# Optimization experiments

Measured on AMD Instinct MI355X. Metric: run time of the kernel, lower is better.

Reference implementation:

```python
import jax, jax.numpy as jnp
import numpy as np

B, S, D_MODEL, HEAD, D_KV = 8, 1024, 1024, 16, 64


def setup_inputs() -> dict:
    key = jax.random.key(0)
    ks = jax.random.split(key, 10)
    std = 1.0 / np.sqrt(D_MODEL)
    inp = {
        "queries": jax.random.normal(ks[0], (B, S, D_MODEL), jnp.float32),
        "keys": jax.random.normal(ks[1], (B, S, D_MODEL), jnp.float32),
        "values": jax.random.normal(ks[2], (B, S, D_MODEL), jnp.float32),
        "group_prob": jax.random.uniform(ks[3], (B, 1, S, S), jnp.float32),
        "attention_mask": jax.random.randint(ks[4], (B, 1, S, S), 0, 2, jnp.int32),
        "Wq": jax.random.normal(ks[5], (HEAD * D_KV, D_MODEL), jnp.float32) * std,
        "bq": jnp.zeros((HEAD * D_KV,), jnp.float32),
        "Wk": jax.random.normal(ks[6], (HEAD * D_KV, D_MODEL), jnp.float32) * std,
        "bk": jnp.zeros((HEAD * D_KV,), jnp.float32),
        "Wv": jax.random.normal(ks[7], (HEAD * D_KV, D_MODEL), jnp.float32) * std,
        "bv": jnp.zeros((HEAD * D_KV,), jnp.float32),
    }
    return inp


def reference(queries, keys, values, group_prob, attention_mask, Wq, bq, Wk, bk, Wv, bv):
    b, nq = queries.shape[:2]
    # QKV projections -> [b, head, seq, d_kv]
    q = (queries @ Wq.T + bq).reshape(b, nq, HEAD, D_KV).transpose(0, 2, 1, 3)
    k = (keys @ Wk.T + bk).reshape(b, -1, HEAD, D_KV).transpose(0, 2, 1, 3)
    v = (values @ Wv.T + bv).reshape(b, -1, HEAD, D_KV).transpose(0, 2, 1, 3)
    # scaled scores [b, head, nq, nk]
    att = jnp.einsum("bhqd,bhkd->bhqk", q, k) / np.sqrt(D_KV).astype(np.float32)
    # NOTE: the original torch code calls att.masked_fill(...) (out-of-place)
    # and discards the result, so attention_mask has no effect. Replicated here.
    att = jax.nn.softmax(att, axis=-1)
    att = att * group_prob  # post-softmax group scaling (breaks fused SDPA)
    out = jnp.einsum("bhqk,bhkd->bhqd", att, v)
    return out.transpose(0, 2, 1, 3).reshape(b, nq, HEAD * D_KV)
```

## Files before the change

kernel.cpp:

```cpp
#include <hip/hip_runtime.h>

#define B_SZ 8
#define S_SZ 1024
#define DM   1024
#define NH   16
#define DK   64

typedef __bf16 bf16;
typedef __bf16 bf16x8 __attribute__((ext_vector_type(8)));
typedef float  f32x4  __attribute__((ext_vector_type(4)));

__device__ __forceinline__ f32x4 mfma16x16x32(bf16x8 a, bf16x8 b, f32x4 c) {
    return __builtin_amdgcn_mfma_f32_16x16x32_bf16(a, b, c, 0, 0, 0);
}

typedef const __attribute__((address_space(1))) void* gptr_t;
typedef __attribute__((address_space(3))) void*       sptr_t;
__device__ __forceinline__ void async_cp16(const void* g, void* s) {
    __builtin_amdgcn_global_load_lds((gptr_t)g, (sptr_t)s, 16, 0, 0);
}

__global__ __launch_bounds__(256)
void cvt_kernel(const float* __restrict__ x0, const float* __restrict__ x1,
                const float* __restrict__ x2, const float* __restrict__ w0,
                const float* __restrict__ w1, const float* __restrict__ w2,
                bf16* __restrict__ xb, bf16* __restrict__ wb)
{
    const int z = blockIdx.y;
    const float* src;
    bf16* dst;
    int n;
    if (z < 3) {
        src = (z == 0) ? x0 : (z == 1) ? x1 : x2;
        dst = xb + (size_t)z * (8u * 1024 * 1024);
        n = 8 * 1024 * 1024;
    } else {
        const int w = z - 3;
        src = (w == 0) ? w0 : (w == 1) ? w1 : w2;
        dst = wb + (size_t)w * (1024 * 1024);
        n = 1024 * 1024;
    }
    const int idx = (blockIdx.x * 256 + threadIdx.x) * 8;
    if (idx >= n) return;
    const float4 a = *(const float4*)(src + idx);
    const float4 c = *(const float4*)(src + idx + 4);
    union { bf16 h[8]; uint4 u; } pk;
    pk.h[0] = (bf16)a.x; pk.h[1] = (bf16)a.y; pk.h[2] = (bf16)a.z; pk.h[3] = (bf16)a.w;
    pk.h[4] = (bf16)c.x; pk.h[5] = (bf16)c.y; pk.h[6] = (bf16)c.z; pk.h[7] = (bf16)c.w;
    *(uint4*)(dst + idx) = pk.u;
}

__global__ __launch_bounds__(256)
void cvt_gp_kernel(const float* __restrict__ gp, bf16* __restrict__ gpb)
{
    const int idx = (blockIdx.x * 256 + threadIdx.x) * 8;
    const float4 a = *(const float4*)(gp + idx);
    const float4 c = *(const float4*)(gp + idx + 4);
    union { bf16 h[8]; uint4 u; } pk;
    pk.h[0] = (bf16)a.x; pk.h[1] = (bf16)a.y; pk.h[2] = (bf16)a.z; pk.h[3] = (bf16)a.w;
    pk.h[4] = (bf16)c.x; pk.h[5] = (bf16)c.y; pk.h[6] = (bf16)c.z; pk.h[7] = (bf16)c.w;
    *(uint4*)(gpb + idx) = pk.u;
}

__global__ __launch_bounds__(256, 2)
void qkv_gemm(const bf16* __restrict__ xb, const bf16* __restrict__ wb,
              const float* __restrict__ bq, const float* __restrict__ bk,
              const float* __restrict__ bv,
              bf16* __restrict__ qb, bf16* __restrict__ kb,
              bf16* __restrict__ vb)
{
    const int z = blockIdx.z;
    const bf16* A  = xb + (size_t)z * (8u * 1024 * 1024);
    const bf16* Bm = wb + (size_t)z * (1024 * 1024);
    const float* bias = (z == 0) ? bq : (z == 1) ? bk : bv;

    __shared__ bf16 Ash[128 * 64];
    __shared__ bf16 Bsh[128 * 64];

    const int tid  = threadIdx.x;
    const int wid  = tid >> 6;
    const int lane = tid & 63;
    const int quad = lane >> 4;
    const int l16  = lane & 15;
    const int wm   = wid >> 1, wn = wid & 1;
    const int bm   = blockIdx.x, bn = blockIdx.y;

    f32x4 acc[4][4] = {};

    for (int k0 = 0; k0 < DM; k0 += 64) {
        __syncthreads();
        #pragma unroll
        for (int i = 0; i < 4; ++i) {
            const int e   = (i * 256 + tid) * 8;
            const int row = e >> 6;
            const int c   = ((e >> 3) & 7) ^ (row & 7);
            async_cp16(A  + (size_t)(bm * 128 + row) * DM + k0 + c * 8, &Ash[e]);
            async_cp16(Bm + (size_t)(bn * 128 + row) * DM + k0 + c * 8, &Bsh[e]);
        }
        __syncthreads();

        #pragma unroll
        for (int ks = 0; ks < 2; ++ks) {
            bf16x8 af[4], bfr[4];
            #pragma unroll
            for (int mi = 0; mi < 4; ++mi) {
                const int row = wm * 64 + mi * 16 + l16;
                af[mi] = *(const bf16x8*)&Ash[row * 64 + (((ks * 4 + quad) ^ (l16 & 7)) << 3)];
            }
            #pragma unroll
            for (int ni = 0; ni < 4; ++ni) {
                const int row = wn * 64 + ni * 16 + l16;
                bfr[ni] = *(const bf16x8*)&Bsh[row * 64 + (((ks * 4 + quad) ^ (l16 & 7)) << 3)];
            }
            #pragma unroll
            for (int mi = 0; mi < 4; ++mi)
                #pragma unroll
                for (int ni = 0; ni < 4; ++ni)
                    acc[mi][ni] = mfma16x16x32(af[mi], bfr[ni], acc[mi][ni]);
        }
    }

    #pragma unroll
    for (int ni = 0; ni < 4; ++ni) {
        const int n    = bn * 128 + wn * 64 + ni * 16 + l16;
        const float bv_ = bias[n];
        const int h = n >> 6, d = n & 63;
        #pragma unroll
        for (int mi = 0; mi < 4; ++mi) {
            const int m0 = bm * 128 + wm * 64 + mi * 16 + quad * 4;
            const int b  = m0 >> 10;
            const int s0 = m0 & 1023;
            if (z == 2) {
                union { bf16 h4[4]; uint2 u; } pk;
                #pragma unroll
                for (int r = 0; r < 4; ++r) pk.h4[r] = (bf16)(acc[mi][ni][r] + bv_);
                *(uint2*)(vb + ((size_t)((b * NH + h) * DK + d)) * S_SZ + s0) = pk.u;
            } else {
                bf16* dst      = (z == 0) ? qb : kb;
                const float sc = (z == 0) ? 0.125f : 1.0f;
                #pragma unroll
                for (int r = 0; r < 4; ++r)
                    dst[((size_t)(b * NH + h) * S_SZ + (s0 + r)) * DK + d] =
                        (bf16)((acc[mi][ni][r] + bv_) * sc);
            }
        }
    }
}

__global__ __launch_bounds__(256, 3)
void attn_kernel(const bf16* __restrict__ qb, const bf16* __restrict__ kb,
                 const bf16* __restrict__ vb, const bf16* __restrict__ gpb,
                 float* __restrict__ out)
{
    __shared__ bf16 Ksh[2][64 * 64];
    __shared__ bf16 Vsh[2][64 * 64];
    __shared__ bf16 Psh[4][16 * 72];
    __shared__ float Lsh[4][16];

    const int tid  = threadIdx.x;
    const int wid  = tid >> 6;
    const int lane = tid & 63;
    const int quad = lane >> 4;
    const int l16  = lane & 15;

    const int bh = blockIdx.x;
    const int qt = blockIdx.y;
    const int b  = bh >> 4;
    const int h  = bh & (NH - 1);
    const int q0 = qt * 64 + wid * 16;

    const bf16* qr = qb + ((size_t)bh * S_SZ + q0 + l16) * DK;
    const bf16x8 qf0 = *(const bf16x8*)(qr + quad * 8);
    const bf16x8 qf1 = *(const bf16x8*)(qr + 32 + quad * 8);

    f32x4 acc[4] = {};
    float lpart = 0.0f;

    const bf16* gpq = gpb + ((size_t)b * S_SZ + q0 + l16) * S_SZ;
    const bf16* kbh = kb + (size_t)bh * (S_SZ * DK);
    const bf16* vbh = vb + (size_t)bh * ((size_t)DK * S_SZ);

    auto STAGE = [&](int t, int bufi) {
        #pragma unroll
        for (int i = 0; i < 2; ++i) {
            const int e   = (i * 256 + tid) * 8;
            const int row = e >> 6;
            const int c   = ((e >> 3) & 7) ^ (row & 7);
            async_cp16(kbh + (size_t)(t * 64 + row) * DK + c * 8, &Ksh[bufi][e]);
        }
        #pragma unroll
        for (int i = 0; i < 2; ++i) {
            const int e   = (i * 256 + tid) * 8;
            const int row = e >> 6;
            const int c   = ((e >> 3) & 7) ^ (row & 7);
            async_cp16(vbh + (size_t)row * S_SZ + t * 64 + c * 8, &Vsh[bufi][e]);
        }
    };
    auto GPLOAD = [&](int t, ushort4 (&g)[4]) {
        #pragma unroll
        for (int nb = 0; nb < 4; ++nb)
            g[nb] = *(const ushort4*)(gpq + t * 64 + nb * 16 + quad * 4);
    };
    auto COMPUTE = [&](const bf16* Kb, const bf16* Vb, const ushort4 (&g)[4]) {
        f32x4 sc[4];
        #pragma unroll
        for (int nb = 0; nb < 4; ++nb) {
            const int row = nb * 16 + l16;
            const bf16x8 kf0 = *(const bf16x8*)&Kb[row * 64 + ((quad ^ (l16 & 7)) << 3)];
            const bf16x8 kf1 = *(const bf16x8*)&Kb[row * 64 + (((4 + quad) ^ (l16 & 7)) << 3)];
            f32x4 s = {0.0f, 0.0f, 0.0f, 0.0f};
            s = mfma16x16x32(kf0, qf0, s);
            s = mfma16x16x32(kf1, qf1, s);
            sc[nb] = s;
        }
        #pragma unroll
        for (int nb = 0; nb < 4; ++nb) {
            union { bf16 h4[4]; uint2 u; } pk;
            const unsigned short* gu = (const unsigned short*)&g[nb];
            #pragma unroll
            for (int r = 0; r < 4; ++r) {
                const float pv = __expf(sc[nb][r]);
                lpart += pv;
                const float gg = __uint_as_float(((unsigned)gu[r]) << 16);
                pk.h4[r] = (bf16)(pv * gg);
            }
            *(uint2*)&Psh[wid][l16 * 72 + nb * 16 + quad * 4] = pk.u;
        }
        bf16x8 pf[2];
        #pragma unroll
        for (int j = 0; j < 2; ++j)
            pf[j] = *(const bf16x8*)&Psh[wid][l16 * 72 + j * 32 + quad * 8];
        #pragma unroll
        for (int ni = 0; ni < 4; ++ni) {
            const int vrow = ni * 16 + l16;
            #pragma unroll
            for (int j = 0; j < 2; ++j) {
                const bf16x8 vf =
                    *(const bf16x8*)&Vb[vrow * 64 + (((j * 4 + quad) ^ (l16 & 7)) << 3)];
                acc[ni] = mfma16x16x32(pf[j], vf, acc[ni]);
            }
        }
    };

    ushort4 gplA[4], gplB[4];
    STAGE(0, 0);
    GPLOAD(0, gplA);
    __syncthreads();

    for (int tt = 0; tt < 8; ++tt) {
        const int t0 = tt * 2;
        STAGE(t0 + 1, 1);
        GPLOAD(t0 + 1, gplB);
        COMPUTE(Ksh[0], Vsh[0], gplA);
        __syncthreads();
        if (t0 + 2 < 16) {
            STAGE(t0 + 2, 0);
            GPLOAD(t0 + 2, gplA);
        }
        COMPUTE(Ksh[1], Vsh[1], gplB);
        __syncthreads();
    }

    lpart += __shfl_xor(lpart, 16, 64);
    lpart += __shfl_xor(lpart, 32, 64);
    if (quad == 0) Lsh[wid][l16] = 1.0f / lpart;
    __syncthreads();

    #pragma unroll
    for (int r = 0; r < 4; ++r) {
        const float inv = Lsh[wid][quad * 4 + r];
        float* orow = out + ((size_t)b * S_SZ + q0 + quad * 4 + r) * DM + h * DK;
        #pragma unroll
        for (int ni = 0; ni < 4; ++ni)
            orow[ni * 16 + l16] = acc[ni][r] * inv;
    }
}

extern "C" void kernel_launch(void* const* d_in, const int* in_sizes, int n_in,
                              void* d_out, int out_size, void* d_ws, size_t ws_size,
                              hipStream_t stream) {
    const float* queries = (const float*)d_in[0];
    const float* keys    = (const float*)d_in[1];
    const float* values  = (const float*)d_in[2];
    const float* gp      = (const float*)d_in[3];
    const float* Wq = (const float*)d_in[5];
    const float* bq = (const float*)d_in[6];
    const float* Wk = (const float*)d_in[7];
    const float* bk = (const float*)d_in[8];
    const float* Wv = (const float*)d_in[9];
    const float* bv = (const float*)d_in[10];
    float* out = (float*)d_out;

    bf16* xb = (bf16*)d_ws;
    bf16* wb = xb + (size_t)3 * 8 * 1024 * 1024;
    bf16* qb = wb + (size_t)3 * 1024 * 1024;
    bf16* kb = qb + (size_t)B_SZ * NH * S_SZ * DK;
    bf16* vb = kb + (size_t)B_SZ * NH * S_SZ * DK;
    bf16* gpb = xb;
    (void)ws_size; (void)in_sizes; (void)n_in; (void)out_size;

    dim3 gc(4096, 6);
    cvt_kernel<<<gc, 256, 0, stream>>>(queries, keys, values, Wq, Wk, Wv, xb, wb);

    dim3 g1(64, 8, 3);
    qkv_gemm<<<g1, 256, 0, stream>>>(xb, wb, bq, bk, bv, qb, kb, vb);

    cvt_gp_kernel<<<dim3(4096), 256, 0, stream>>>(gp, gpb);

    dim3 g2(B_SZ * NH , S_SZ / 64 , 1);
    attn_kernel<<<g2, 256, 0, stream>>>(qb, kb, vb, gpb, out);
}
```

Before: 354.3 us.

## Process two 16-row query tiles per wave to reuse K/V fragments

```diff
diff --git a/kernel.cpp b/kernel.cpp
--- a/kernel.cpp
+++ b/kernel.cpp
@@ -154,8 +154,8 @@
 {
     __shared__ bf16 Ksh[2][64 * 64];
     __shared__ bf16 Vsh[2][64 * 64];
-    __shared__ bf16 Psh[4][16 * 72];
-    __shared__ float Lsh[4][16];
+    __shared__ bf16 Psh[4][32 * 72];
+    __shared__ float Lsh[4][32];
 
     const int tid  = threadIdx.x;
     const int wid  = tid >> 6;
@@ -167,16 +167,21 @@
     const int qt = blockIdx.y;
     const int b  = bh >> 4;
     const int h  = bh & (NH - 1);
-    const int q0 = qt * 64 + wid * 16;
-
-    const bf16* qr = qb + ((size_t)bh * S_SZ + q0 + l16) * DK;
-    const bf16x8 qf0 = *(const bf16x8*)(qr + quad * 8);
-    const bf16x8 qf1 = *(const bf16x8*)(qr + 32 + quad * 8);
-
-    f32x4 acc[4] = {};
-    float lpart = 0.0f;
-
-    const bf16* gpq = gpb + ((size_t)b * S_SZ + q0 + l16) * S_SZ;
+    const int q0 = qt * 128 + wid * 32;
+
+    bf16x8 qf[2][2];
+    #pragma unroll
+    for (int mq = 0; mq < 2; ++mq) {
+        const bf16* qr = qb + ((size_t)bh * S_SZ + q0 + mq * 16 + l16) * DK;
+        qf[mq][0] = *(const bf16x8*)(qr + quad * 8);
+        qf[mq][1] = *(const bf16x8*)(qr + 32 + quad * 8);
+    }
+
+    f32x4 acc[2][4] = {};
+    float lpart[2] = {};
+
+    const bf16* gpq0 = gpb + ((size_t)b * S_SZ + q0 + l16) * S_SZ;
+    const bf16* gpq1 = gpq0 + (size_t)16 * S_SZ;
     const bf16* kbh = kb + (size_t)bh * (S_SZ * DK);
     const bf16* vbh = vb + (size_t)bh * ((size_t)DK * S_SZ);
 
@@ -196,40 +201,42 @@
             async_cp16(vbh + (size_t)row * S_SZ + t * 64 + c * 8, &Vsh[bufi][e]);
         }
     };
-    auto GPLOAD = [&](int t, ushort4 (&g)[4]) {
-        #pragma unroll
-        for (int nb = 0; nb < 4; ++nb)
-            g[nb] = *(const ushort4*)(gpq + t * 64 + nb * 16 + quad * 4);
+    auto GPLOAD = [&](int t, ushort4 (&g)[2][4]) {
+        #pragma unroll
+        for (int nb = 0; nb < 4; ++nb) {
+            g[0][nb] = *(const ushort4*)(gpq0 + t * 64 + nb * 16 + quad * 4);
+            g[1][nb] = *(const ushort4*)(gpq1 + t * 64 + nb * 16 + quad * 4);
+        }
     };
-    auto COMPUTE = [&](const bf16* Kb, const bf16* Vb, const ushort4 (&g)[4]) {
-        f32x4 sc[4];
+    auto COMPUTE = [&](const bf16* Kb, const bf16* Vb, const ushort4 (&g)[2][4]) {
         #pragma unroll
         for (int nb = 0; nb < 4; ++nb) {
             const int row = nb * 16 + l16;
             const bf16x8 kf0 = *(const bf16x8*)&Kb[row * 64 + ((quad ^ (l16 & 7)) << 3)];
             const bf16x8 kf1 = *(const bf16x8*)&Kb[row * 64 + (((4 + quad) ^ (l16 & 7)) << 3)];
-            f32x4 s = {0.0f, 0.0f, 0.0f, 0.0f};
-            s = mfma16x16x32(kf0, qf0, s);
-            s = mfma16x16x32(kf1, qf1, s);
-            sc[nb] = s;
-        }
-        #pragma unroll
-        for (int nb = 0; nb < 4; ++nb) {
-            union { bf16 h4[4]; uint2 u; } pk;
-            const unsigned short* gu = (const unsigned short*)&g[nb];
-            #pragma unroll
-            for (int r = 0; r < 4; ++r) {
-                const float pv = __expf(sc[nb][r]);
-                lpart += pv;
-                const float gg = __uint_as_float(((unsigned)gu[r]) << 16);
-                pk.h4[r] = (bf16)(pv * gg);
-            }
-            *(uint2*)&Psh[wid][l16 * 72 + nb * 16 + quad * 4] = pk.u;
-        }
-        bf16x8 pf[2];
-        #pragma unroll
-        for (int j = 0; j < 2; ++j)
-            pf[j] = *(const bf16x8*)&Psh[wid][l16 * 72 + j * 32 + quad * 8];
+            #pragma unroll
+            for (int mq = 0; mq < 2; ++mq) {
+                f32x4 s = {0.0f, 0.0f, 0.0f, 0.0f};
+                s = mfma16x16x32(kf0, qf[mq][0], s);
+                s = mfma16x16x32(kf1, qf[mq][1], s);
+                union { bf16 h4[4]; uint2 u; } pk;
+                const unsigned short* gu = (const unsigned short*)&g[mq][nb];
+                #pragma unroll
+                for (int r = 0; r < 4; ++r) {
+                    const float pv = __expf(s[r]);
+                    lpart[mq] += pv;
+                    const float gg = __uint_as_float(((unsigned)gu[r]) << 16);
+                    pk.h4[r] = (bf16)(pv * gg);
+                }
+                *(uint2*)&Psh[wid][(mq * 16 + l16) * 72 + nb * 16 + quad * 4] = pk.u;
+            }
+        }
+        bf16x8 pf[2][2];
+        #pragma unroll
+        for (int mq = 0; mq < 2; ++mq)
+            #pragma unroll
+            for (int j = 0; j < 2; ++j)
+                pf[mq][j] = *(const bf16x8*)&Psh[wid][(mq * 16 + l16) * 72 + j * 32 + quad * 8];
         #pragma unroll
         for (int ni = 0; ni < 4; ++ni) {
             const int vrow = ni * 16 + l16;
@@ -237,12 +244,14 @@
             for (int j = 0; j < 2; ++j) {
                 const bf16x8 vf =
                     *(const bf16x8*)&Vb[vrow * 64 + (((j * 4 + quad) ^ (l16 & 7)) << 3)];
-                acc[ni] = mfma16x16x32(pf[j], vf, acc[ni]);
+                #pragma unroll
+                for (int mq = 0; mq < 2; ++mq)
+                    acc[mq][ni] = mfma16x16x32(pf[mq][j], vf, acc[mq][ni]);
             }
         }
     };
 
-    ushort4 gplA[4], gplB[4];
+    ushort4 gplA[2][4], gplB[2][4];
     STAGE(0, 0);
     GPLOAD(0, gplA);
     __syncthreads();
@@ -261,18 +270,25 @@
         __syncthreads();
     }
 
-    lpart += __shfl_xor(lpart, 16, 64);
-    lpart += __shfl_xor(lpart, 32, 64);
-    if (quad == 0) Lsh[wid][l16] = 1.0f / lpart;
+    #pragma unroll
+    for (int mq = 0; mq < 2; ++mq) {
+        float lp = lpart[mq];
+        lp += __shfl_xor(lp, 16, 64);
+        lp += __shfl_xor(lp, 32, 64);
+        if (quad == 0) Lsh[wid][mq * 16 + l16] = 1.0f / lp;
+    }
     __syncthreads();
 
     #pragma unroll
-    for (int r = 0; r < 4; ++r) {
-        const float inv = Lsh[wid][quad * 4 + r];
-        float* orow = out + ((size_t)b * S_SZ + q0 + quad * 4 + r) * DM + h * DK;
-        #pragma unroll
-        for (int ni = 0; ni < 4; ++ni)
-            orow[ni * 16 + l16] = acc[ni][r] * inv;
+    for (int mq = 0; mq < 2; ++mq) {
+        #pragma unroll
+        for (int r = 0; r < 4; ++r) {
+            const float inv = Lsh[wid][mq * 16 + quad * 4 + r];
+            float* orow = out + ((size_t)b * S_SZ + q0 + mq * 16 + quad * 4 + r) * DM + h * DK;
+            #pragma unroll
+            for (int ni = 0; ni < 4; ++ni)
+                orow[ni * 16 + l16] = acc[mq][ni][r] * inv;
+        }
     }
 }
 
@@ -307,6 +323,6 @@
 
     cvt_gp_kernel<<<dim3(4096), 256, 0, stream>>>(gp, gpb);
 
-    dim3 g2(B_SZ * NH , S_SZ / 64 , 1);
+    dim3 g2(B_SZ * NH , S_SZ / 128 , 1);
     attn_kernel<<<g2, 256, 0, stream>>>(qb, kb, vb, gpb, out);
 }
```

Result: no change. 352.8 us (-0.4%).
